# Optimization experiments

Measured on AMD Instinct MI355X. Metric: run time of the kernel, lower is better.

The kernel has to match this reference:

```python
import jax, jax.numpy as jnp
import numpy as np

N, C_IN, C_B, H, W, POOL = 2, 256, 128, 100, 100, 10
HW = H * W


def conv1x1(x, w, b):
    # x: [n,c,h,w], w: [o,c] -> [n,o,h,w]
    return jnp.einsum('nchw,oc->nohw', x, w) + b[None, :, None, None]


def instance_norm(x, eps=1e-5):
    # torch InstanceNorm2d(affine=False): normalize per (n,c) over spatial dims
    m = jnp.mean(x, axis=(2, 3), keepdims=True)
    v = jnp.var(x, axis=(2, 3), keepdims=True)
    return (x - m) * jax.lax.rsqrt(v + eps)


def bilinear_sample(feat, x, y, h, w):
    # feat: [n,c,h*w]; x,y: [n,p] sample coords. mmcv bilinear_interpolate semantics.
    valid = (x >= -1.0) & (x <= w) & (y >= -1.0) & (y <= h)
    x = jnp.maximum(x, 0.0)
    y = jnp.maximum(y, 0.0)
    x0f = jnp.floor(x)
    y0f = jnp.floor(y)
    cx = x0f >= w - 1
    cy = y0f >= h - 1
    x0 = jnp.where(cx, float(w - 1), x0f).astype(jnp.int32)
    y0 = jnp.where(cy, float(h - 1), y0f).astype(jnp.int32)
    x1 = jnp.minimum(x0 + 1, w - 1)
    y1 = jnp.minimum(y0 + 1, h - 1)
    xe = jnp.where(cx, x0.astype(x.dtype), x)
    ye = jnp.where(cy, y0.astype(y.dtype), y)
    lx = xe - x0
    ly = ye - y0
    hx = 1.0 - lx
    hy = 1.0 - ly

    def g(iy, ix):
        return jnp.take_along_axis(feat, (iy * w + ix)[:, None, :], axis=2)  # [n,c,p]

    val = ((hy * hx)[:, None] * g(y0, x0) + (hy * lx)[:, None] * g(y0, x1)
           + (ly * hx)[:, None] * g(y1, x0) + (ly * lx)[:, None] * g(y1, x1))
    return val * valid[:, None]


def border_align(feat, boxes, pool_size, c):
    # feat: [n,4c,h,w]; boxes: [n,hw,4]; returns [n,hw,4,c]
    n, _, h, w = feat.shape
    hw = boxes.shape[1]
    k = pool_size + 1
    t = jnp.arange(k, dtype=feat.dtype) / pool_size  # [k]
    x1, y1, x2, y2 = boxes[..., 0], boxes[..., 1], boxes[..., 2], boxes[..., 3]
    bw = x2 - x1
    bh = y2 - y1
    feat4 = feat.reshape(n, 4, c, h * w)
    # border order (mmcv): top, left, bottom, right
    xs_t = x1[..., None] + t * bw[..., None]
    ys_t = jnp.broadcast_to(y1[..., None], xs_t.shape)
    ys_l = y1[..., None] + t * bh[..., None]
    xs_l = jnp.broadcast_to(x1[..., None], ys_l.shape)
    xs_b = xs_t
    ys_b = jnp.broadcast_to(y2[..., None], xs_t.shape)
    ys_r = ys_l
    xs_r = jnp.broadcast_to(x2[..., None], ys_l.shape)
    outs = []
    for b, (xs, ys) in enumerate([(xs_t, ys_t), (xs_l, ys_l), (xs_b, ys_b), (xs_r, ys_r)]):
        v = bilinear_sample(feat4[:, b], xs.reshape(n, -1), ys.reshape(n, -1), h, w)  # [n,c,hw*k]
        outs.append(v.reshape(n, c, hw, k).max(axis=-1))  # max-pool over border points
    out = jnp.stack(outs, axis=3)  # [n,c,hw,4]
    return jnp.transpose(out, (0, 2, 3, 1))  # [n,hw,4,c]


def setup_inputs():
    key = jax.random.key(0)
    ks = jax.random.split(key, 9)
    feature = jax.random.normal(ks[0], (N, C_IN, H, W), jnp.float32)
    u = jax.random.uniform(ks[1], (N, HW, 4), jnp.float32)
    x1 = u[..., 0] * (W * 0.5)
    y1 = u[..., 1] * (H * 0.5)
    x2 = x1 + 1.0 + u[..., 2] * (W * 0.5 - 1.0)
    y2 = y1 + 1.0 + u[..., 3] * (H * 0.5 - 1.0)
    boxes = jnp.stack([x1, y1, x2, y2], axis=-1)
    wh = jax.random.uniform(ks[2], (N, HW, 2), jnp.float32) * W
    s1 = 1.0 / np.sqrt(C_IN).astype(np.float32)
    w_cur = jax.random.normal(ks[3], (C_B, C_IN), jnp.float32) * s1
    b_cur = jax.random.normal(ks[4], (C_B,), jnp.float32) * 0.01
    w_ltrb = jax.random.normal(ks[5], (4 * C_B, C_IN), jnp.float32) * s1
    b_ltrb = jax.random.normal(ks[6], (4 * C_B,), jnp.float32) * 0.01
    s2 = 1.0 / np.sqrt(5 * C_B).astype(np.float32)
    w_out = jax.random.normal(ks[7], (C_IN, 5 * C_B), jnp.float32) * s2
    b_out = jax.random.normal(ks[8], (C_IN,), jnp.float32) * 0.01
    return {"feature": feature, "boxes": boxes, "wh": wh,
            "w_cur": w_cur, "b_cur": b_cur, "w_ltrb": w_ltrb, "b_ltrb": b_ltrb,
            "w_out": w_out, "b_out": b_out}


def reference(feature, boxes, wh, w_cur, b_cur, w_ltrb, b_ltrb, w_out, b_out):
    n, _, h, w = feature.shape
    fm_short = jax.nn.relu(instance_norm(conv1x1(feature, w_cur, b_cur)))          # [n,C_B,h,w]
    ltrb = jax.nn.relu(instance_norm(conv1x1(feature, w_ltrb, b_ltrb)))            # [n,4*C_B,h,w]
    aligned = border_align(ltrb, boxes, POOL, C_B)                                  # [n,hw,4,C_B]
    # faithful to torch: permute(0,3,1,2).reshape(N,-1,H,W)
    aligned = jnp.transpose(aligned, (0, 3, 1, 2)).reshape(n, -1, h, w)             # [n,4*C_B,h,w]
    cat = jnp.concatenate([aligned, fm_short], axis=1)                              # [n,5*C_B,h,w]
    return jax.nn.relu(conv1x1(cat, w_out, b_out))                                  # [n,C_IN,h,w]
```

## Files before the change

### kernel.cpp

```cpp
#include <hip/hip_runtime.h>
#include <hip/hip_bf16.h>
#include <math.h>

#define NB    2
#define CIN   256
#define CB    128
#define HH    100
#define WW    100
#define NPIX  10000
#define CH1   640
#define K2    640
#define O2    256
#define NM    40000
#define NSAMP 11

typedef __attribute__((ext_vector_type(8))) short bf16x8;
typedef __attribute__((ext_vector_type(4))) float f32x4;
typedef unsigned short ushort_t;

__device__ __forceinline__ unsigned short f2bf(float f) {
    unsigned u = __float_as_uint(f);
    u += 0x7FFF + ((u >> 16) & 1);
    return (unsigned short)(u >> 16);
}
__device__ __forceinline__ float bf2f(ushort_t u) {
    return __uint_as_float(((unsigned)u) << 16);
}

#define MFMA16(a, b, c) __builtin_amdgcn_mfma_f32_16x16x32_bf16((a), (b), (c), 0, 0, 0)

__global__ __launch_bounds__(256) void prep_k(const float* __restrict__ wcur,
                                              const float* __restrict__ wltrb,
                                              const float* __restrict__ wout,
                                              ushort_t* __restrict__ W1b,
                                              ushort_t* __restrict__ W2b) {
    int id = blockIdx.x * 256 + threadIdx.x;
    if (id < CH1 * CIN) {
        const int ch = id / CIN;
        const float v = (ch < CB) ? wcur[id] : wltrb[id - CB * CIN];
        W1b[id] = f2bf(v);
        return;
    }
    id -= CH1 * CIN;
    if (id < O2 * K2) {
        const int o = id / K2, k = id % K2;
        const int korig = (k < 512) ? ((k & 127) * 4 + (k >> 7)) : k;
        W2b[id] = f2bf(wout[(size_t)o * K2 + korig]);
    }
}

__global__ __launch_bounds__(256) void featT_k(const float* __restrict__ feat,
                                               ushort_t* __restrict__ featTb) {
    __shared__ float T[128][65];
    const int pix0 = blockIdx.x * 64;
    const int ch0  = blockIdx.y * 128;
    const int n    = blockIdx.z;
    const int tid  = threadIdx.x;
    {
        const int pl = tid & 63, cl0 = tid >> 6;
#pragma unroll
        for (int i = 0; i < 32; ++i) {
            const int cl = cl0 + i * 4;
            const int pix = pix0 + pl;
            T[cl][pl] = (pix < NPIX)
                ? feat[((size_t)n * CIN + ch0 + cl) * NPIX + pix] : 0.f;
        }
    }
    __syncthreads();
    const int cl = tid & 127, pl0 = tid >> 7;
#pragma unroll
    for (int j = 0; j < 32; ++j) {
        const int pp = pl0 + j * 2;
        const int pix = pix0 + pp;
        if (pix < NPIX)
            featTb[((size_t)n * NPIX + pix) * CIN + ch0 + cl] = f2bf(T[cl][pp]);
    }
}

__global__ __launch_bounds__(256) void gemm1T_k(const ushort_t* __restrict__ featTb,
                                                const ushort_t* __restrict__ W1b,
                                                ushort_t* __restrict__ rawT,
                                                float* __restrict__ st) {
    __shared__ ushort_t Bs[2][128][40];
    const int pix0 = blockIdx.x * 128;
    const int ch0  = blockIdx.y * 128;
    const int n    = blockIdx.z;
    const int tid  = threadIdx.x;
    const int lane = tid & 63, wv = tid >> 6;
    const int wp = wv & 1, wc = wv >> 1;
    const int l15 = lane & 15, lg = lane >> 4;

    f32x4 acc[4][4];
#pragma unroll
    for (int am = 0; am < 4; ++am)
#pragma unroll
        for (int bn = 0; bn < 4; ++bn)
#pragma unroll
            for (int r = 0; r < 4; ++r) acc[am][bn][r] = 0.f;

    const int srow = tid >> 1, spart = tid & 1;
    const int spix = pix0 + srow;
    const ushort_t* Bsrc  = featTb + (size_t)n * NPIX * CIN;
    const ushort_t* Wbase = W1b + (size_t)(ch0 + wc * 64 + l15) * CIN + lg * 8;

    uint4 pv0, pv1, pv2, pv3;
    {
        pv0 = make_uint4(0, 0, 0, 0); pv1 = pv0; pv2 = pv0; pv3 = pv0;
        if (spix < NPIX) {
            const ushort_t* s = Bsrc + (size_t)spix * CIN + spart * 16;
            pv0 = *(const uint4*)s;       pv1 = *(const uint4*)(s + 8);
            pv2 = *(const uint4*)(s + 32); pv3 = *(const uint4*)(s + 40);
        }
    }
#pragma unroll
    for (int ks = 0; ks < CIN / 64; ++ks) {
        *(uint4*)&Bs[0][srow][spart * 16]     = pv0;
        *(uint4*)&Bs[0][srow][spart * 16 + 8] = pv1;
        *(uint4*)&Bs[1][srow][spart * 16]     = pv2;
        *(uint4*)&Bs[1][srow][spart * 16 + 8] = pv3;
        __syncthreads();
        if (ks + 1 < CIN / 64) {
            pv0 = make_uint4(0, 0, 0, 0); pv1 = pv0; pv2 = pv0; pv3 = pv0;
            if (spix < NPIX) {
                const ushort_t* s = Bsrc + (size_t)spix * CIN + (ks + 1) * 64 + spart * 16;
                pv0 = *(const uint4*)s;       pv1 = *(const uint4*)(s + 8);
                pv2 = *(const uint4*)(s + 32); pv3 = *(const uint4*)(s + 40);
            }
        }
#pragma unroll
        for (int half = 0; half < 2; ++half) {
            const int k0 = ks * 64 + half * 32;
            bf16x8 bfrag[4];
#pragma unroll
            for (int bn = 0; bn < 4; ++bn)
                bfrag[bn] = *(const bf16x8*)(Wbase + (size_t)bn * 16 * CIN + k0);
#pragma unroll
            for (int am = 0; am < 4; ++am) {
                const bf16x8 a = *(const bf16x8*)&Bs[half][wp * 64 + am * 16 + l15][lg * 8];
#pragma unroll
                for (int bn = 0; bn < 4; ++bn)
                    acc[am][bn] = MFMA16(a, bfrag[bn], acc[am][bn]);
            }
        }
        __syncthreads();
    }

#pragma unroll
    for (int bn = 0; bn < 4; ++bn) {
        float s = 0.f, q = 0.f;
#pragma unroll
        for (int am = 0; am < 4; ++am)
#pragma unroll
            for (int r = 0; r < 4; ++r) { const float v = acc[am][bn][r]; s += v; q += v * v; }
        s += __shfl_xor(s, 16); q += __shfl_xor(q, 16);
        s += __shfl_xor(s, 32); q += __shfl_xor(q, 32);
        if (lg == 0) {
            const int ch = ch0 + wc * 64 + bn * 16 + l15;
            atomicAdd(&st[(size_t)(n * CH1 + ch) * 2],     s);
            atomicAdd(&st[(size_t)(n * CH1 + ch) * 2 + 1], q);
        }
    }

#pragma unroll
    for (int am = 0; am < 4; ++am)
#pragma unroll
        for (int r = 0; r < 4; ++r) {
            const int pix = pix0 + wp * 64 + am * 16 + lg * 4 + r;
            if (pix < NPIX) {
                ushort_t* dst = rawT + (size_t)(n * NPIX + pix) * CH1 + ch0 + wc * 64 + l15;
#pragma unroll
                for (int bn = 0; bn < 4; ++bn) dst[bn * 16] = f2bf(acc[am][bn][r]);
            }
        }
}

__global__ __launch_bounds__(256) void stfin_k(const float* __restrict__ st,
                                               float2* __restrict__ MS) {
    const int ch = blockIdx.x * 256 + threadIdx.x;
    if (ch >= NB * CH1) return;
    const float sum = st[(size_t)ch * 2];
    const float sq  = st[(size_t)ch * 2 + 1];
    const float m   = sum * (1.0f / (float)NPIX);
    const float var = fmaxf(sq * (1.0f / (float)NPIX) - m * m, 0.f);
    MS[ch] = make_float2(m, 1.0f / sqrtf(var + 1e-5f));
}

__global__ __launch_bounds__(256) void normAll_k(const ushort_t* __restrict__ rawT,
                                                 const float2* __restrict__ MS,
                                                 ushort_t* __restrict__ CATb,
                                                 ushort_t* __restrict__ Lb) {
    const int id = blockIdx.x * 256 + threadIdx.x;
    if (id >= NB * NPIX * 80) return;
    const int c8 = (id % 80) * 8;
    const int np = id / 80;
    const int n = np / NPIX, pix = np % NPIX;
    const uint4 v = *(const uint4*)(rawT + (size_t)np * CH1 + c8);
    ushort_t tmp[8]; *(uint4*)tmp = v;
    ushort_t outv[8];
    const float2* msb = MS + n * CH1 + c8;
#pragma unroll
    for (int j = 0; j < 8; ++j) {
        const float2 ms = msb[j];
        const float x = (bf2f(tmp[j]) - ms.x) * ms.y;
        outv[j] = f2bf(fmaxf(x, 0.f));
    }
    ushort_t* dst;
    if (c8 < 128) {
        dst = CATb + ((size_t)(n * 5 + 4) * NPIX + pix) * 128 + c8;
    } else {
        const int b  = (c8 - 128) >> 7;
        const int cc = (c8 - 128) & 127;
        dst = Lb + ((size_t)((n * 4 + b) * NPIX) + pix) * 128 + cc;
    }
    *(uint4*)dst = *(uint4*)outv;
}

__global__ __launch_bounds__(256) void coord_k(const float* __restrict__ boxes,
                                               int* __restrict__ OFFS,
                                               float4* __restrict__ WTS) {
    const int id = blockIdx.x * 256 + threadIdx.x;
    if (id >= NB * NM * NSAMP) return;
    const int k  = id % NSAMP;
    const int mm = id / NSAMP;
    const int m  = mm % NM;
    const int n  = mm / NM;
    const int p = m >> 2, b = m & 3;
    const float* bx = boxes + ((size_t)n * NPIX + p) * 4;
    const float x1 = bx[0], y1 = bx[1], x2 = bx[2], y2 = bx[3];
    const float bw = __fsub_rn(x2, x1), bh = __fsub_rn(y2, y1);
    const float t = __fdiv_rn((float)k, 10.0f);
    float x, y;
    if (b == 0)      { x = __fadd_rn(x1, __fmul_rn(t, bw)); y = y1; }
    else if (b == 1) { x = x1; y = __fadd_rn(y1, __fmul_rn(t, bh)); }
    else if (b == 2) { x = __fadd_rn(x1, __fmul_rn(t, bw)); y = y2; }
    else             { x = x2; y = __fadd_rn(y1, __fmul_rn(t, bh)); }
    const bool valid = (x >= -1.f) && (x <= (float)WW) && (y >= -1.f) && (y <= (float)HH);
    x = fmaxf(x, 0.f); y = fmaxf(y, 0.f);
    const float x0f = floorf(x), y0f = floorf(y);
    const bool cx = (x0f >= (float)(WW - 1));
    const bool cy = (y0f >= (float)(HH - 1));
    const int ix0 = cx ? (WW - 1) : (int)x0f;
    const int iy0 = cy ? (HH - 1) : (int)y0f;
    const int ix1 = min(ix0 + 1, WW - 1);
    const int iy1 = min(iy0 + 1, HH - 1);
    const float lx = cx ? 0.f : __fsub_rn(x, (float)ix0);
    const float ly = cy ? 0.f : __fsub_rn(y, (float)iy0);
    const float hx = 1.f - lx, hy = 1.f - ly;
    const float vf = valid ? 1.f : 0.f;
    const int dx = ix1 - ix0, dy = iy1 - iy0;
    const int did = (((n * 4 + b) * NPIX) + p) * NSAMP + k;
    OFFS[did] = (iy0 * WW + ix0) | (dx << 14) | (dy << 15);
    WTS[did]  = make_float4((hy * hx) * vf, (hy * lx) * vf,
                            (ly * hx) * vf, (ly * lx) * vf);
}

__global__ __launch_bounds__(256) void borderB_k(const int* __restrict__ OFFS,
                                                 const float4* __restrict__ WTS,
                                                 const ushort_t* __restrict__ Lb,
                                                 ushort_t* __restrict__ CATb) {
    const int s = blockIdx.x & 7;
    const int n = s >> 2, b = s & 3;
    const int u = threadIdx.x >> 4;
    const int c8 = (threadIdx.x & 15) * 8;
    const int p = (blockIdx.x >> 3) * 16 + u;
    const ushort_t* Lbase = Lb + ((size_t)(n * 4 + b) * NPIX) * 128 + c8;
    const int dbase = (((n * 4 + b) * NPIX) + p) * NSAMP;
    float a0 = -INFINITY, a1 = -INFINITY, a2 = -INFINITY, a3 = -INFINITY;
    float a4 = -INFINITY, a5 = -INFINITY, a6 = -INFINITY, a7 = -INFINITY;
#pragma unroll
    for (int k = 0; k < NSAMP; ++k) {
        const int    v  = OFFS[dbase + k];
        const float4 wt = WTS[dbase + k];
        const int off = v & 0x3FFF;
        const int dxo = ((v >> 14) & 1) * 128;
        const int dyo = ((v >> 15) & 1) * (WW * 128);
        const ushort_t* t = Lbase + (size_t)off * 128;
        ushort_t g00[8], g01[8], g10[8], g11[8];
        *(uint4*)g00 = *(const uint4*)(t);
        *(uint4*)g01 = *(const uint4*)(t + dxo);
        *(uint4*)g10 = *(const uint4*)(t + dyo);
        *(uint4*)g11 = *(const uint4*)(t + dyo + dxo);
#define TAPJ(j, accv)                                                        \
        {                                                                    \
            float val = wt.x * bf2f(g00[j]);                                 \
            val = fmaf(wt.y, bf2f(g01[j]), val);                             \
            val = fmaf(wt.z, bf2f(g10[j]), val);                             \
            val = fmaf(wt.w, bf2f(g11[j]), val);                             \
            accv = fmaxf(accv, val);                                         \
        }
        TAPJ(0, a0) TAPJ(1, a1) TAPJ(2, a2) TAPJ(3, a3)
        TAPJ(4, a4) TAPJ(5, a5) TAPJ(6, a6) TAPJ(7, a7)
#undef TAPJ
    }
    const int m = p * 4 + b;
    ushort_t outv[8];
    outv[0] = f2bf(a0); outv[1] = f2bf(a1); outv[2] = f2bf(a2); outv[3] = f2bf(a3);
    outv[4] = f2bf(a4); outv[5] = f2bf(a5); outv[6] = f2bf(a6); outv[7] = f2bf(a7);
    *(uint4*)(CATb + ((size_t)n * 5 * NPIX + m) * 128 + c8) = *(uint4*)outv;
}

__global__ __launch_bounds__(256) void gemm2_k(const ushort_t* __restrict__ W2b,
                                               const ushort_t* __restrict__ CATb,
                                               const float* __restrict__ bout,
                                               float* __restrict__ out) {
    __shared__ ushort_t Bs[2][128][40];
    const int pix0 = blockIdx.x * 128;
    const int o0   = blockIdx.y * 64;
    const int n    = blockIdx.z;
    const int tid  = threadIdx.x;
    const int lane = tid & 63, wv = tid >> 6;
    const int wo = wv & 1, wp = wv >> 1;
    const int l15 = lane & 15, lg = lane >> 4;

    f32x4 acc[2][4];
#pragma unroll
    for (int am = 0; am < 2; ++am)
#pragma unroll
        for (int bn = 0; bn < 4; ++bn)
#pragma unroll
            for (int r = 0; r < 4; ++r) acc[am][bn][r] = 0.f;

    const int srow = tid >> 1, spart = tid & 1;
    const int spix = pix0 + srow;
    const ushort_t* CATn = CATb + (size_t)n * 5 * NPIX * 128;
    const ushort_t* A0 = W2b + (size_t)(o0 + wo * 32 + l15) * K2 + lg * 8;
    const ushort_t* A1 = A0 + 16 * K2;

#define G2ADDR(j) (CATn + ((size_t)((j) >> 2) * NPIX + spix) * 128 + (((j) & 3) * 32) + spart * 16)

    uint4 pv0, pv1, pv2, pv3;
    {
        pv0 = make_uint4(0, 0, 0, 0); pv1 = pv0; pv2 = pv0; pv3 = pv0;
        if (spix < NPIX) {
            const ushort_t* s0 = G2ADDR(0);
            const ushort_t* s1 = G2ADDR(1);
            pv0 = *(const uint4*)s0; pv1 = *(const uint4*)(s0 + 8);
            pv2 = *(const uint4*)s1; pv3 = *(const uint4*)(s1 + 8);
        }
    }
#pragma unroll
    for (int ks = 0; ks < K2 / 64; ++ks) {
        *(uint4*)&Bs[0][srow][spart * 16]     = pv0;
        *(uint4*)&Bs[0][srow][spart * 16 + 8] = pv1;
        *(uint4*)&Bs[1][srow][spart * 16]     = pv2;
        *(uint4*)&Bs[1][srow][spart * 16 + 8] = pv3;
        __syncthreads();
        if (ks + 1 < K2 / 64) {
            pv0 = make_uint4(0, 0, 0, 0); pv1 = pv0; pv2 = pv0; pv3 = pv0;
            if (spix < NPIX) {
                const ushort_t* s0 = G2ADDR(2 * ks + 2);
                const ushort_t* s1 = G2ADDR(2 * ks + 3);
                pv0 = *(const uint4*)s0; pv1 = *(const uint4*)(s0 + 8);
                pv2 = *(const uint4*)s1; pv3 = *(const uint4*)(s1 + 8);
            }
        }
#pragma unroll
        for (int half = 0; half < 2; ++half) {
            const int k0 = ks * 64 + half * 32;
            const bf16x8 af0 = *(const bf16x8*)(A0 + k0);
            const bf16x8 af1 = *(const bf16x8*)(A1 + k0);
#pragma unroll
            for (int bn = 0; bn < 4; ++bn) {
                const bf16x8 bfr = *(const bf16x8*)&Bs[half][wp * 64 + bn * 16 + l15][lg * 8];
                acc[0][bn] = MFMA16(af0, bfr, acc[0][bn]);
                acc[1][bn] = MFMA16(af1, bfr, acc[1][bn]);
            }
        }
        __syncthreads();
    }
#undef G2ADDR

    const int obase = o0 + wo * 32 + lg * 4;
#pragma unroll
    for (int am = 0; am < 2; ++am) {
        const float4 bi = *(const float4*)&bout[obase + am * 16];
#pragma unroll
        for (int bn = 0; bn < 4; ++bn) {
            const int pix = pix0 + wp * 64 + bn * 16 + l15;
            if (pix < NPIX) {
                float* dst = out + ((size_t)n * O2 + obase + am * 16) * NPIX + pix;
                dst[0 * (size_t)NPIX] = fmaxf(acc[am][bn][0] + bi.x, 0.f);
                dst[1 * (size_t)NPIX] = fmaxf(acc[am][bn][1] + bi.y, 0.f);
                dst[2 * (size_t)NPIX] = fmaxf(acc[am][bn][2] + bi.z, 0.f);
                dst[3 * (size_t)NPIX] = fmaxf(acc[am][bn][3] + bi.w, 0.f);
            }
        }
    }
}

extern "C" void kernel_launch(void* const* d_in, const int* in_sizes, int n_in,
                              void* d_out, int out_size, void* d_ws, size_t ws_size,
                              hipStream_t stream) {
    const float* feature = (const float*)d_in[0];
    const float* boxes   = (const float*)d_in[1];
    const float* w_cur   = (const float*)d_in[3];
    const float* w_ltrb  = (const float*)d_in[5];
    const float* w_out   = (const float*)d_in[7];
    const float* b_out   = (const float*)d_in[8];
    float* out = (float*)d_out;

    float* ws = (float*)d_ws;
    float*    st     = ws;
    float2*   MS     = (float2*)(st + NB * CH1 * 2);
    ushort_t* featTb = (ushort_t*)(MS + NB * CH1);
    ushort_t* rawT   = featTb + (size_t)NB * NPIX * CIN;
    ushort_t* CATb   = rawT + (size_t)NB * NPIX * CH1;
    ushort_t* Lb     = CATb + (size_t)NB * 5 * NPIX * 128;
    ushort_t* W1b    = Lb + (size_t)NB * 4 * NPIX * 128;
    ushort_t* W2b    = W1b + CH1 * CIN;
    int*      OFFS   = (int*)(W2b + O2 * K2);
    float4*   WTS    = (float4*)(OFFS + NB * NM * NSAMP);

    hipMemsetAsync(st, 0, (size_t)NB * CH1 * 2 * sizeof(float), stream);
    prep_k<<<(CH1 * CIN + O2 * K2 + 255) / 256, 256, 0, stream>>>(w_cur, w_ltrb, w_out, W1b, W2b);
    featT_k<<<dim3((NPIX + 63) / 64, 2, NB), 256, 0, stream>>>(feature, featTb);
    gemm1T_k<<<dim3((NPIX + 127) / 128, CH1 / 128, NB), 256, 0, stream>>>(featTb, W1b, rawT, st);
    stfin_k<<<(NB * CH1 + 255) / 256, 256, 0, stream>>>(st, MS);
    normAll_k<<<(NB * NPIX * 80 + 255) / 256, 256, 0, stream>>>(rawT, MS, CATb, Lb);
    coord_k<<<(NB * NM * NSAMP + 255) / 256, 256, 0, stream>>>(boxes, OFFS, WTS);
    borderB_k<<<NB * 4 * NPIX / 16, 256, 0, stream>>>(OFFS, WTS, Lb, CATb);
    gemm2_k<<<dim3((NPIX + 127) / 128, O2 / 64, NB), 256, 0, stream>>>(W2b, CATb, b_out, out);
}
```

Measured before the change: 221.8 us.

## Drop LDS staging in both GEMMs and use packed fp16 border sampling

Both MFMA GEMMs stop staging activation tiles through shared memory with barriers and instead load each bf16 fragment straight from global memory. The transposed feature buffer is padded to a multiple of 128 pixels, with zero-filled padding rows, so gemm1 can read without bounds checks. The ltrb maps feeding border_align are now stored as fp16, and the bilinear max-pool uses packed half2 FMA and max instead of per-element fp32 math. The intent is to remove LDS traffic and sync overhead and halve the ALU work in the sampling kernel. In exchange it relies on L1/L2 caching for fragment reuse across waves and accepts fp16 rounding in the border accumulation.

```diff
diff --git a/kernel.cpp b/kernel.cpp
--- a/kernel.cpp
+++ b/kernel.cpp
@@ -8,6 +8,7 @@
 #define HH    100
 #define WW    100
 #define NPIX  10000
+#define NPIXP 10112
 #define CH1   640
 #define K2    640
 #define O2    256
@@ -16,6 +17,7 @@
 
 typedef __attribute__((ext_vector_type(8))) short bf16x8;
 typedef __attribute__((ext_vector_type(4))) float f32x4;
+typedef _Float16 h2 __attribute__((ext_vector_type(2)));
 typedef unsigned short ushort_t;
 
 __device__ __forceinline__ unsigned short f2bf(float f) {
@@ -72,8 +74,8 @@
     for (int j = 0; j < 32; ++j) {
         const int pp = pl0 + j * 2;
         const int pix = pix0 + pp;
-        if (pix < NPIX)
-            featTb[((size_t)n * NPIX + pix) * CIN + ch0 + cl] = f2bf(T[cl][pp]);
+        if (pix < NPIXP)
+            featTb[((size_t)n * NPIXP + pix) * CIN + ch0 + cl] = f2bf(T[cl][pp]);
     }
 }
 
@@ -81,7 +83,6 @@
                                                 const ushort_t* __restrict__ W1b,
                                                 ushort_t* __restrict__ rawT,
                                                 float* __restrict__ st) {
-    __shared__ ushort_t Bs[2][128][40];
     const int pix0 = blockIdx.x * 128;
     const int ch0  = blockIdx.y * 128;
     const int n    = blockIdx.z;
@@ -98,51 +99,24 @@
 #pragma unroll
             for (int r = 0; r < 4; ++r) acc[am][bn][r] = 0.f;
 
-    const int srow = tid >> 1, spart = tid & 1;
-    const int spix = pix0 + srow;
-    const ushort_t* Bsrc  = featTb + (size_t)n * NPIX * CIN;
+    const ushort_t* Abase = featTb + ((size_t)n * NPIXP + pix0 + wp * 64 + l15) * CIN + lg * 8;
     const ushort_t* Wbase = W1b + (size_t)(ch0 + wc * 64 + l15) * CIN + lg * 8;
 
-    uint4 pv0, pv1, pv2, pv3;
-    {
-        pv0 = make_uint4(0, 0, 0, 0); pv1 = pv0; pv2 = pv0; pv3 = pv0;
-        if (spix < NPIX) {
-            const ushort_t* s = Bsrc + (size_t)spix * CIN + spart * 16;
-            pv0 = *(const uint4*)s;       pv1 = *(const uint4*)(s + 8);
-            pv2 = *(const uint4*)(s + 32); pv3 = *(const uint4*)(s + 40);
-        }
-    }
-#pragma unroll
-    for (int ks = 0; ks < CIN / 64; ++ks) {
-        *(uint4*)&Bs[0][srow][spart * 16]     = pv0;
-        *(uint4*)&Bs[0][srow][spart * 16 + 8] = pv1;
-        *(uint4*)&Bs[1][srow][spart * 16]     = pv2;
-        *(uint4*)&Bs[1][srow][spart * 16 + 8] = pv3;
-        __syncthreads();
-        if (ks + 1 < CIN / 64) {
-            pv0 = make_uint4(0, 0, 0, 0); pv1 = pv0; pv2 = pv0; pv3 = pv0;
-            if (spix < NPIX) {
-                const ushort_t* s = Bsrc + (size_t)spix * CIN + (ks + 1) * 64 + spart * 16;
-                pv0 = *(const uint4*)s;       pv1 = *(const uint4*)(s + 8);
-                pv2 = *(const uint4*)(s + 32); pv3 = *(const uint4*)(s + 40);
-            }
-        }
-#pragma unroll
-        for (int half = 0; half < 2; ++half) {
-            const int k0 = ks * 64 + half * 32;
-            bf16x8 bfrag[4];
+#pragma unroll
+    for (int ks = 0; ks < CIN / 32; ++ks) {
+        const int k0 = ks * 32;
+        bf16x8 afrag[4], bfrag[4];
+#pragma unroll
+        for (int am = 0; am < 4; ++am)
+            afrag[am] = *(const bf16x8*)(Abase + (size_t)am * 16 * CIN + k0);
+#pragma unroll
+        for (int bn = 0; bn < 4; ++bn)
+            bfrag[bn] = *(const bf16x8*)(Wbase + (size_t)bn * 16 * CIN + k0);
+#pragma unroll
+        for (int am = 0; am < 4; ++am)
 #pragma unroll
             for (int bn = 0; bn < 4; ++bn)
-                bfrag[bn] = *(const bf16x8*)(Wbase + (size_t)bn * 16 * CIN + k0);
-#pragma unroll
-            for (int am = 0; am < 4; ++am) {
-                const bf16x8 a = *(const bf16x8*)&Bs[half][wp * 64 + am * 16 + l15][lg * 8];
-#pragma unroll
-                for (int bn = 0; bn < 4; ++bn)
-                    acc[am][bn] = MFMA16(a, bfrag[bn], acc[am][bn]);
-            }
-        }
-        __syncthreads();
+                acc[am][bn] = MFMA16(afrag[am], bfrag[bn], acc[am][bn]);
     }
 
 #pragma unroll
@@ -188,7 +162,7 @@
 __global__ __launch_bounds__(256) void normAll_k(const ushort_t* __restrict__ rawT,
                                                  const float2* __restrict__ MS,
                                                  ushort_t* __restrict__ CATb,
-                                                 ushort_t* __restrict__ Lb) {
+                                                 ushort_t* __restrict__ Lh) {
     const int id = blockIdx.x * 256 + threadIdx.x;
     if (id >= NB * NPIX * 80) return;
     const int c8 = (id % 80) * 8;
@@ -196,23 +170,29 @@
     const int n = np / NPIX, pix = np % NPIX;
     const uint4 v = *(const uint4*)(rawT + (size_t)np * CH1 + c8);
     ushort_t tmp[8]; *(uint4*)tmp = v;
-    ushort_t outv[8];
     const float2* msb = MS + n * CH1 + c8;
-#pragma unroll
-    for (int j = 0; j < 8; ++j) {
-        const float2 ms = msb[j];
-        const float x = (bf2f(tmp[j]) - ms.x) * ms.y;
-        outv[j] = f2bf(fmaxf(x, 0.f));
-    }
-    ushort_t* dst;
     if (c8 < 128) {
-        dst = CATb + ((size_t)(n * 5 + 4) * NPIX + pix) * 128 + c8;
+        ushort_t outv[8];
+#pragma unroll
+        for (int j = 0; j < 8; ++j) {
+            const float2 ms = msb[j];
+            const float x = (bf2f(tmp[j]) - ms.x) * ms.y;
+            outv[j] = f2bf(fmaxf(x, 0.f));
+        }
+        *(uint4*)(CATb + ((size_t)(n * 5 + 4) * NPIX + pix) * 128 + c8) = *(uint4*)outv;
     } else {
+        _Float16 outh[8];
+#pragma unroll
+        for (int j = 0; j < 8; ++j) {
+            const float2 ms = msb[j];
+            const float x = (bf2f(tmp[j]) - ms.x) * ms.y;
+            outh[j] = (_Float16)fmaxf(x, 0.f);
+        }
         const int b  = (c8 - 128) >> 7;
         const int cc = (c8 - 128) & 127;
-        dst = Lb + ((size_t)((n * 4 + b) * NPIX) + pix) * 128 + cc;
-    }
-    *(uint4*)dst = *(uint4*)outv;
+        ushort_t* dst = Lh + ((size_t)((n * 4 + b) * NPIX) + pix) * 128 + cc;
+        *(uint4*)dst = *(uint4*)outh;
+    }
 }
 
 __global__ __launch_bounds__(256) void coord_k(const float* __restrict__ boxes,
@@ -254,19 +234,18 @@
                             (ly * hx) * vf, (ly * lx) * vf);
 }
 
-__global__ __launch_bounds__(256) void borderB_k(const int* __restrict__ OFFS,
+__global__ __launch_bounds__(256) void borderH_k(const int* __restrict__ OFFS,
                                                  const float4* __restrict__ WTS,
-                                                 const ushort_t* __restrict__ Lb,
+                                                 const ushort_t* __restrict__ Lh,
                                                  ushort_t* __restrict__ CATb) {
     const int s = blockIdx.x & 7;
     const int n = s >> 2, b = s & 3;
     const int u = threadIdx.x >> 4;
     const int c8 = (threadIdx.x & 15) * 8;
     const int p = (blockIdx.x >> 3) * 16 + u;
-    const ushort_t* Lbase = Lb + ((size_t)(n * 4 + b) * NPIX) * 128 + c8;
+    const ushort_t* Lbase = Lh + ((size_t)(n * 4 + b) * NPIX) * 128 + c8;
     const int dbase = (((n * 4 + b) * NPIX) + p) * NSAMP;
-    float a0 = -INFINITY, a1 = -INFINITY, a2 = -INFINITY, a3 = -INFINITY;
-    float a4 = -INFINITY, a5 = -INFINITY, a6 = -INFINITY, a7 = -INFINITY;
+    h2 acc0 = (h2)0, acc1 = (h2)0, acc2 = (h2)0, acc3 = (h2)0;
 #pragma unroll
     for (int k = 0; k < NSAMP; ++k) {
         const int    v  = OFFS[dbase + k];
@@ -275,27 +254,32 @@
         const int dxo = ((v >> 14) & 1) * 128;
         const int dyo = ((v >> 15) & 1) * (WW * 128);
         const ushort_t* t = Lbase + (size_t)off * 128;
-        ushort_t g00[8], g01[8], g10[8], g11[8];
+        h2 g00[4], g01[4], g10[4], g11[4];
         *(uint4*)g00 = *(const uint4*)(t);
         *(uint4*)g01 = *(const uint4*)(t + dxo);
         *(uint4*)g10 = *(const uint4*)(t + dyo);
         *(uint4*)g11 = *(const uint4*)(t + dyo + dxo);
-#define TAPJ(j, accv)                                                        \
-        {                                                                    \
-            float val = wt.x * bf2f(g00[j]);                                 \
-            val = fmaf(wt.y, bf2f(g01[j]), val);                             \
-            val = fmaf(wt.z, bf2f(g10[j]), val);                             \
-            val = fmaf(wt.w, bf2f(g11[j]), val);                             \
-            accv = fmaxf(accv, val);                                         \
-        }
-        TAPJ(0, a0) TAPJ(1, a1) TAPJ(2, a2) TAPJ(3, a3)
-        TAPJ(4, a4) TAPJ(5, a5) TAPJ(6, a6) TAPJ(7, a7)
+        const _Float16 s00 = (_Float16)wt.x, s01 = (_Float16)wt.y;
+        const _Float16 s10 = (_Float16)wt.z, s11 = (_Float16)wt.w;
+        const h2 w00 = (h2){s00, s00}, w01 = (h2){s01, s01};
+        const h2 w10 = (h2){s10, s10}, w11 = (h2){s11, s11};
+#define TAPJ(j, accv)                                                         \
+        {                                                                     \
+            h2 val = w00 * g00[j];                                            \
+            val = __builtin_elementwise_fma(w01, g01[j], val);                \
+            val = __builtin_elementwise_fma(w10, g10[j], val);                \
+            val = __builtin_elementwise_fma(w11, g11[j], val);                \
+            accv = __builtin_elementwise_max(accv, val);                      \
+        }
+        TAPJ(0, acc0) TAPJ(1, acc1) TAPJ(2, acc2) TAPJ(3, acc3)
 #undef TAPJ
     }
     const int m = p * 4 + b;
     ushort_t outv[8];
-    outv[0] = f2bf(a0); outv[1] = f2bf(a1); outv[2] = f2bf(a2); outv[3] = f2bf(a3);
-    outv[4] = f2bf(a4); outv[5] = f2bf(a5); outv[6] = f2bf(a6); outv[7] = f2bf(a7);
+    outv[0] = f2bf((float)acc0.x); outv[1] = f2bf((float)acc0.y);
+    outv[2] = f2bf((float)acc1.x); outv[3] = f2bf((float)acc1.y);
+    outv[4] = f2bf((float)acc2.x); outv[5] = f2bf((float)acc2.y);
+    outv[6] = f2bf((float)acc3.x); outv[7] = f2bf((float)acc3.y);
     *(uint4*)(CATb + ((size_t)n * 5 * NPIX + m) * 128 + c8) = *(uint4*)outv;
 }
 
@@ -303,7 +287,6 @@
                                                const ushort_t* __restrict__ CATb,
                                                const float* __restrict__ bout,
                                                float* __restrict__ out) {
-    __shared__ ushort_t Bs[2][128][40];
     const int pix0 = blockIdx.x * 128;
     const int o0   = blockIdx.y * 64;
     const int n    = blockIdx.z;
@@ -320,55 +303,25 @@
 #pragma unroll
             for (int r = 0; r < 4; ++r) acc[am][bn][r] = 0.f;
 
-    const int srow = tid >> 1, spart = tid & 1;
-    const int spix = pix0 + srow;
     const ushort_t* CATn = CATb + (size_t)n * 5 * NPIX * 128;
     const ushort_t* A0 = W2b + (size_t)(o0 + wo * 32 + l15) * K2 + lg * 8;
     const ushort_t* A1 = A0 + 16 * K2;
-
-#define G2ADDR(j) (CATn + ((size_t)((j) >> 2) * NPIX + spix) * 128 + (((j) & 3) * 32) + spart * 16)
-
-    uint4 pv0, pv1, pv2, pv3;
-    {
-        pv0 = make_uint4(0, 0, 0, 0); pv1 = pv0; pv2 = pv0; pv3 = pv0;
-        if (spix < NPIX) {
-            const ushort_t* s0 = G2ADDR(0);
-            const ushort_t* s1 = G2ADDR(1);
-            pv0 = *(const uint4*)s0; pv1 = *(const uint4*)(s0 + 8);
-            pv2 = *(const uint4*)s1; pv3 = *(const uint4*)(s1 + 8);
-        }
-    }
-#pragma unroll
-    for (int ks = 0; ks < K2 / 64; ++ks) {
-        *(uint4*)&Bs[0][srow][spart * 16]     = pv0;
-        *(uint4*)&Bs[0][srow][spart * 16 + 8] = pv1;
-        *(uint4*)&Bs[1][srow][spart * 16]     = pv2;
-        *(uint4*)&Bs[1][srow][spart * 16 + 8] = pv3;
-        __syncthreads();
-        if (ks + 1 < K2 / 64) {
-            pv0 = make_uint4(0, 0, 0, 0); pv1 = pv0; pv2 = pv0; pv3 = pv0;
-            if (spix < NPIX) {
-                const ushort_t* s0 = G2ADDR(2 * ks + 2);
-                const ushort_t* s1 = G2ADDR(2 * ks + 3);
-                pv0 = *(const uint4*)s0; pv1 = *(const uint4*)(s0 + 8);
-                pv2 = *(const uint4*)s1; pv3 = *(const uint4*)(s1 + 8);
-            }
-        }
-#pragma unroll
-        for (int half = 0; half < 2; ++half) {
-            const int k0 = ks * 64 + half * 32;
-            const bf16x8 af0 = *(const bf16x8*)(A0 + k0);
-            const bf16x8 af1 = *(const bf16x8*)(A1 + k0);
-#pragma unroll
-            for (int bn = 0; bn < 4; ++bn) {
-                const bf16x8 bfr = *(const bf16x8*)&Bs[half][wp * 64 + bn * 16 + l15][lg * 8];
-                acc[0][bn] = MFMA16(af0, bfr, acc[0][bn]);
-                acc[1][bn] = MFMA16(af1, bfr, acc[1][bn]);
-            }
-        }
-        __syncthreads();
-    }
-#undef G2ADDR
+    const ushort_t* Bbase = CATn + ((size_t)(pix0 + wp * 64 + l15)) * 128 + lg * 8;
+
+#pragma unroll
+    for (int ks = 0; ks < K2 / 32; ++ks) {
+        const int k0 = ks * 32;
+        const int slot = k0 >> 7, c0 = k0 & 127;
+        const bf16x8 af0 = *(const bf16x8*)(A0 + k0);
+        const bf16x8 af1 = *(const bf16x8*)(A1 + k0);
+#pragma unroll
+        for (int bn = 0; bn < 4; ++bn) {
+            const bf16x8 bfr = *(const bf16x8*)(Bbase
+                + ((size_t)slot * NPIX + (size_t)bn * 16) * 128 + c0);
+            acc[0][bn] = MFMA16(af0, bfr, acc[0][bn]);
+            acc[1][bn] = MFMA16(af1, bfr, acc[1][bn]);
+        }
+    }
 
     const int obase = o0 + wo * 32 + lg * 4;
 #pragma unroll
@@ -403,21 +356,21 @@
     float*    st     = ws;
     float2*   MS     = (float2*)(st + NB * CH1 * 2);
     ushort_t* featTb = (ushort_t*)(MS + NB * CH1);
-    ushort_t* rawT   = featTb + (size_t)NB * NPIX * CIN;
+    ushort_t* rawT   = featTb + (size_t)NB * NPIXP * CIN;
     ushort_t* CATb   = rawT + (size_t)NB * NPIX * CH1;
-    ushort_t* Lb     = CATb + (size_t)NB * 5 * NPIX * 128;
-    ushort_t* W1b    = Lb + (size_t)NB * 4 * NPIX * 128;
+    ushort_t* Lh     = CATb + (size_t)NB * 5 * NPIX * 128;
+    ushort_t* W1b    = Lh + (size_t)NB * 4 * NPIX * 128;
     ushort_t* W2b    = W1b + CH1 * CIN;
     int*      OFFS   = (int*)(W2b + O2 * K2);
     float4*   WTS    = (float4*)(OFFS + NB * NM * NSAMP);
 
-    hipMemsetAsync(st, 0, (size_t)NB * CH1 * 2 * sizeof(float), stream);
+    (void)hipMemsetAsync(st, 0, (size_t)NB * CH1 * 2 * sizeof(float), stream);
     prep_k<<<(CH1 * CIN + O2 * K2 + 255) / 256, 256, 0, stream>>>(w_cur, w_ltrb, w_out, W1b, W2b);
-    featT_k<<<dim3((NPIX + 63) / 64, 2, NB), 256, 0, stream>>>(feature, featTb);
-    gemm1T_k<<<dim3((NPIX + 127) / 128, CH1 / 128, NB), 256, 0, stream>>>(featTb, W1b, rawT, st);
+    featT_k<<<dim3(NPIXP / 64, 2, NB), 256, 0, stream>>>(feature, featTb);
+    gemm1T_k<<<dim3(NPIXP / 128, CH1 / 128, NB), 256, 0, stream>>>(featTb, W1b, rawT, st);
     stfin_k<<<(NB * CH1 + 255) / 256, 256, 0, stream>>>(st, MS);
-    normAll_k<<<(NB * NPIX * 80 + 255) / 256, 256, 0, stream>>>(rawT, MS, CATb, Lb);
+    normAll_k<<<(NB * NPIX * 80 + 255) / 256, 256, 0, stream>>>(rawT, MS, CATb, Lh);
     coord_k<<<(NB * NM * NSAMP + 255) / 256, 256, 0, stream>>>(boxes, OFFS, WTS);
-    borderB_k<<<NB * 4 * NPIX / 16, 256, 0, stream>>>(OFFS, WTS, Lb, CATb);
+    borderH_k<<<NB * 4 * NPIX / 16, 256, 0, stream>>>(OFFS, WTS, Lh, CATb);
     gemm2_k<<<dim3((NPIX + 127) / 128, O2 / 64, NB), 256, 0, stream>>>(W2b, CATb, b_out, out);
 }
```

After: 246.6 us. 11.2% more time.
